# Performance work log

Hardware: AMD Instinct MI355X
Metric: run time of the kernel (lower is better)

Reference implementation:

```python
import jax, jax.numpy as jnp
import numpy as np

B, S, D, H, HID = 8192, 16, 128, 8, 1024
DH = D // H  # 16
GCN, NUMF = 40, 103
EPS = 1e-5

def _make_pe():
    pos = np.arange(S, dtype=np.float64)[:, None]
    i = np.arange(D, dtype=np.float64)[None, :]
    pe = pos / np.power(10000.0, (i // 2 * 2.0) / D)
    pe[:, 0::2] = np.sin(pe[:, 0::2])
    pe[:, 1::2] = np.cos(pe[:, 1::2])
    return jnp.asarray(pe, dtype=jnp.float32)  # [S, D]

PE = _make_pe()

def setup_inputs() -> dict:
    key = jax.random.key(0)
    ks = jax.random.split(key, 16)
    rn = lambda k, shape, s=0.02: (jax.random.normal(k, shape, jnp.float32) * s)
    return {
        "x": jax.random.normal(ks[0], (B, S, D), jnp.float32),
        "gcn_i": jax.random.normal(ks[1], (B, GCN), jnp.float32),
        "num": jax.random.normal(ks[2], (B, NUMF), jnp.float32),
        # two independent encoder layers, params stacked on leading dim
        "Wq": rn(ks[3], (2, D, D)), "bq": jnp.zeros((2, D), jnp.float32),
        "Wk": rn(ks[4], (2, D, D)), "bk": jnp.zeros((2, D), jnp.float32),
        "Wv": rn(ks[5], (2, D, D)), "bv": jnp.zeros((2, D), jnp.float32),
        "Wo": rn(ks[6], (2, D, D)), "bo": jnp.zeros((2, D), jnp.float32),
        "ln1_g": jnp.ones((2, D), jnp.float32), "ln1_b": jnp.zeros((2, D), jnp.float32),
        "W1": rn(ks[7], (2, D, HID)), "b1": jnp.zeros((2, HID), jnp.float32),
        "W2": rn(ks[8], (2, HID, D)), "b2": jnp.zeros((2, D), jnp.float32),
        "ln2_g": jnp.ones((2, D), jnp.float32), "ln2_b": jnp.zeros((2, D), jnp.float32),
        # head
        "Wn": rn(ks[9], (NUMF, D)), "bnum": jnp.zeros((D,), jnp.float32),
        "bn_gamma": jnp.ones((D,), jnp.float32), "bn_beta": jnp.zeros((D,), jnp.float32),
        "Wf": rn(ks[10], (S * D + GCN + D, 1)), "bf": jnp.zeros((1,), jnp.float32),
    }

def _ln(x, g, b):
    m = x.mean(-1, keepdims=True)
    v = ((x - m) ** 2).mean(-1, keepdims=True)
    return (x - m) * jax.lax.rsqrt(v + EPS) * g + b

def reference(x, gcn_i, num, Wq, bq, Wk, bk, Wv, bv, Wo, bo, ln1_g, ln1_b,
              W1, b1, W2, b2, ln2_g, ln2_b, Wn, bnum, bn_gamma, bn_beta, Wf, bf):
    out = x + PE  # positional encoding (dropout = identity in eval)
    scale = DH ** -0.5
    for l in range(2):
        # NOTE: original uses a raw .view(B*H, -1, DH) (no transpose) -- faithful reshape
        q = (out @ Wq[l] + bq[l]).reshape(B * H, S, DH)
        k = (out @ Wk[l] + bk[l]).reshape(B * H, S, DH)
        v = (out @ Wv[l] + bv[l]).reshape(B * H, S, DH)
        attn = jax.nn.softmax(jnp.einsum('nsd,ntd->nst', q, k) * scale, axis=-1)
        ctx = jnp.einsum('nst,ntd->nsd', attn, v).reshape(B, S, D)
        h = _ln(ctx @ Wo[l] + bo[l] + out, ln1_g[l], ln1_b[l])
        ff = jax.nn.relu(h @ W1[l] + b1[l]) @ W2[l] + b2[l]
        out = _ln(ff + h, ln2_g[l], ln2_b[l])
    flat = out.reshape(B, S * D)  # [B, 2048]
    n = num @ Wn + bnum  # [B, 128]
    # BatchNorm1d, training-mode forward (biased batch variance)
    mu = n.mean(0)
    var = ((n - mu) ** 2).mean(0)
    n = (n - mu) * jax.lax.rsqrt(var + EPS) * bn_gamma + bn_beta
    p = jnp.concatenate([flat, gcn_i, n], axis=-1)  # [B, 2216]
    return jax.nn.sigmoid(p @ Wf + bf)
```

## Files before the change

kernel.cpp:

```cpp
#include <hip/hip_runtime.h>
#include <hip/hip_bf16.h>
#include <math.h>

#define B_SZ   8192
#define S_SZ   16
#define D_SZ   128
#define HID_SZ 1024
#define NUMF_SZ 103
#define GCN_SZ 40
#define G_B    4
#define NBLK   (B_SZ / G_B)
#define STRD   136

typedef short bh8 __attribute__((ext_vector_type(8)));
typedef float fx4 __attribute__((ext_vector_type(4)));
typedef unsigned short us4 __attribute__((ext_vector_type(4)));

__device__ __forceinline__ fx4 mfma16(bh8 a, bh8 b, fx4 c) {
    return __builtin_amdgcn_mfma_f32_16x16x32_bf16(a, b, c, 0, 0, 0);
}

__device__ __forceinline__ unsigned short f2b(float f) {
    union { __hip_bfloat16 b; unsigned short u; } cv;
    cv.b = __float2bfloat16(f);
    return cv.u;
}
__device__ __forceinline__ float bu2f(unsigned short u) {
    return __uint_as_float(((unsigned)u) << 16);
}

__global__ __launch_bounds__(256) void prep_weights(
    const float* __restrict__ Wq, const float* __restrict__ Wk,
    const float* __restrict__ Wv, const float* __restrict__ Wo,
    const float* __restrict__ W1, const float* __restrict__ W2,
    unsigned short* __restrict__ WswQ, unsigned short* __restrict__ WswK,
    unsigned short* __restrict__ WswV, unsigned short* __restrict__ WswO,
    unsigned short* __restrict__ Wsw1, unsigned short* __restrict__ Wsw2,
    float* __restrict__ PEt)
{
    int i = blockIdx.x * 256 + threadIdx.x;
    if (i < 2048) {
        int s = i >> 7, c = i & 127;
        float expo = (float)((c >> 1) * 2) * (1.0f / 128.0f);
        float denom = powf(10000.0f, expo);
        float ang = (float)s / denom;
        PEt[i] = (c & 1) ? cosf(ang) : sinf(ang);
    }
    if (i < 2 * 16384) {
        int l = i >> 14, r = i & 16383;
        int nt = r >> 11, ks = (r >> 9) & 3, lane = (r >> 3) & 63, e = r & 7;
        int k = ks * 32 + (lane >> 4) * 8 + e;
        int n = nt * 16 + (lane & 15);
        int s = l * 16384 + k * 128 + n;
        WswQ[i] = f2b(Wq[s]); WswK[i] = f2b(Wk[s]);
        WswV[i] = f2b(Wv[s]); WswO[i] = f2b(Wo[s]);
    }
    {
        int l = i >> 17, r = i & 131071;
        int nt = r >> 11, ks = (r >> 9) & 3, lane = (r >> 3) & 63, e = r & 7;
        int k = ks * 32 + (lane >> 4) * 8 + e;
        int n = nt * 16 + (lane & 15);
        Wsw1[i] = f2b(W1[l * 131072 + k * 1024 + n]);
    }
    {
        int l = i >> 17, r = i & 131071;
        int nt = r >> 14, kt = (r >> 9) & 31, lane = (r >> 3) & 63, e = r & 7;
        int k = kt * 32 + (lane >> 4) * 8 + e;
        int n = nt * 16 + (lane & 15);
        Wsw2[i] = f2b(W2[l * 131072 + k * 128 + n]);
    }
}

__global__ __launch_bounds__(256, 2) void encoder_fused(
    const float* __restrict__ x, const float* __restrict__ gcn,
    const float* __restrict__ bq, const float* __restrict__ bk,
    const float* __restrict__ bv, const float* __restrict__ bo,
    const float* __restrict__ ln1g, const float* __restrict__ ln1b,
    const float* __restrict__ b1, const float* __restrict__ b2p,
    const float* __restrict__ ln2g, const float* __restrict__ ln2b,
    const float* __restrict__ Wf,
    const unsigned short* __restrict__ WswQ, const unsigned short* __restrict__ WswK,
    const unsigned short* __restrict__ WswV, const unsigned short* __restrict__ WswO,
    const unsigned short* __restrict__ Wsw1, const unsigned short* __restrict__ Wsw2,
    const float* __restrict__ PEt,
    float* __restrict__ acc1)
{
    __shared__ unsigned short ACT[64][STRD];
    __shared__ unsigned short Qb[64][STRD];
    __shared__ unsigned short Kb[64][STRD];
    __shared__ unsigned short Vb[64][STRD];
    __shared__ float2 LNp2[64][4];
    __shared__ float LNs[64][2];
    __shared__ unsigned short Pb[4][16][16];

    unsigned short* Vb4 = &Vb[0][0];

    const int t = threadIdx.x;
    const int w = t >> 6, lane = t & 63;
    const int q = lane >> 4, ln = lane & 15;
    const int bbase = blockIdx.x * G_B;

    {
        const float4* xb = (const float4*)(x + (size_t)bbase * 2048);
        const float4* pe4 = (const float4*)PEt;
#pragma unroll
        for (int i = 0; i < 8; ++i) {
            int f4 = i * 256 + t;
            float4 xv = xb[f4];
            float4 pv = pe4[f4 & 511];
            int flat = f4 * 4;
            int row = flat >> 7, col = flat & 127;
            ushort4 pk = {f2b(xv.x + pv.x), f2b(xv.y + pv.y),
                          f2b(xv.z + pv.z), f2b(xv.w + pv.w)};
            *(ushort4*)&ACT[row][col] = pk;
        }
    }
    __syncthreads();

    for (int l = 0; l < 2; ++l) {
        {
            bh8 afr[4][4];
#pragma unroll
            for (int mt = 0; mt < 4; ++mt)
#pragma unroll
                for (int ks = 0; ks < 4; ++ks)
                    afr[mt][ks] = *(const bh8*)&ACT[mt * 16 + ln][ks * 32 + q * 8];
#pragma unroll
            for (int mtx = 0; mtx < 2; ++mtx) {
                const unsigned short* Wm = (mtx == 0) ? WswQ + l * 16384 : WswK + l * 16384;
                const float* bias = (mtx == 0) ? bq + l * 128 : bk + l * 128;
                unsigned short (*dst)[STRD] = (mtx == 0) ? Qb : Kb;
#pragma unroll
                for (int i2 = 0; i2 < 2; ++i2) {
                    int nt = w * 2 + i2;
                    bh8 wfr[4];
#pragma unroll
                    for (int ks = 0; ks < 4; ++ks)
                        wfr[ks] = *(const bh8*)(Wm + ((nt * 4 + ks) * 64 + lane) * 8);
                    int n0 = nt * 16 + q * 4;
                    fx4 bb4 = *(const fx4*)&bias[n0];
#pragma unroll
                    for (int mt = 0; mt < 4; ++mt) {
                        fx4 acc = {0.f, 0.f, 0.f, 0.f};
#pragma unroll
                        for (int ks = 0; ks < 4; ++ks) acc = mfma16(wfr[ks], afr[mt][ks], acc);
                        us4 o;
#pragma unroll
                        for (int r2 = 0; r2 < 4; ++r2) o[r2] = f2b(acc[r2] + bb4[r2]);
                        *(us4*)&dst[mt * 16 + ln][n0] = o;
                    }
                }
            }
#pragma unroll
            for (int i2 = 0; i2 < 2; ++i2) {
                int nt = w * 2 + i2;
                bh8 wfr[4];
#pragma unroll
                for (int ks = 0; ks < 4; ++ks)
                    wfr[ks] = *(const bh8*)(WswV + l * 16384 + ((nt * 4 + ks) * 64 + lane) * 8);
                int n = nt * 16 + ln;
                float bb = bv[l * 128 + n];
#pragma unroll
                for (int mt = 0; mt < 4; ++mt) {
                    fx4 acc = {0.f, 0.f, 0.f, 0.f};
#pragma unroll
                    for (int ks = 0; ks < 4; ++ks) acc = mfma16(afr[mt][ks], wfr[ks], acc);
#pragma unroll
                    for (int r2 = 0; r2 < 4; ++r2) {
                        int s = q * 4 + r2;
                        Vb4[(((mt * 8 + (s >> 1)) * 16) + ln) * 16 +
                            (((s & 1) << 3) | nt)] = f2b(acc[r2] + bb);
                    }
                }
            }
        }
        __syncthreads();

        {
            const int E = w;
            const int rbase = E * 16 + (ln >> 3);
            const int ccol = (ln & 7) * 16;
#pragma unroll
            for (int g = 0; g < 8; ++g) {
                bh8 kfr = 0, qfr = 0;
                if (q < 2) {
                    kfr = *(const bh8*)&Kb[rbase + 2 * g][ccol + q * 8];
                    qfr = *(const bh8*)&Qb[rbase + 2 * g][ccol + q * 8];
                }
                fx4 st = mfma16(kfr, qfr, fx4{0.f, 0.f, 0.f, 0.f});
                float p0 = st[0] * 0.25f, p1 = st[1] * 0.25f;
                float p2 = st[2] * 0.25f, p3 = st[3] * 0.25f;
                float mx = fmaxf(fmaxf(p0, p1), fmaxf(p2, p3));
                mx = fmaxf(mx, __shfl_xor(mx, 16));
                mx = fmaxf(mx, __shfl_xor(mx, 32));
                p0 = __expf(p0 - mx); p1 = __expf(p1 - mx);
                p2 = __expf(p2 - mx); p3 = __expf(p3 - mx);
                float sm = (p0 + p1) + (p2 + p3);
                sm += __shfl_xor(sm, 16);
                sm += __shfl_xor(sm, 32);
                float is = 1.0f / sm;
                ushort4 pk = {f2b(p0 * is), f2b(p1 * is), f2b(p2 * is), f2b(p3 * is)};
                *(ushort4*)&Pb[w][ln][q * 4] = pk;
                bh8 vfr = 0, pfr = 0;
                if (q < 2) {
                    vfr = *(const bh8*)&Vb4[(((E * 8 + g) * 16) + ln) * 16 + q * 8];
                    pfr = *(const bh8*)&Pb[w][ln][q * 8];
                }
                fx4 cx = mfma16(vfr, pfr, fx4{0.f, 0.f, 0.f, 0.f});
                ushort4 ck = {f2b(cx[0]), f2b(cx[1]), f2b(cx[2]), f2b(cx[3])};
                *(ushort4*)&Qb[rbase + 2 * g][ccol + q * 4] = ck;
            }
        }
        __syncthreads();

        fx4 Cv[2][4];
        {
            bh8 cfr[4][4];
#pragma unroll
            for (int mt = 0; mt < 4; ++mt)
#pragma unroll
                for (int ks = 0; ks < 4; ++ks)
                    cfr[mt][ks] = *(const bh8*)&Qb[mt * 16 + ln][ks * 32 + q * 8];
#pragma unroll
            for (int i2 = 0; i2 < 2; ++i2) {
                int nt = w * 2 + i2, n0 = nt * 16 + q * 4;
                bh8 wfr[4];
#pragma unroll
                for (int ks = 0; ks < 4; ++ks)
                    wfr[ks] = *(const bh8*)(WswO + l * 16384 + ((nt * 4 + ks) * 64 + lane) * 8);
                fx4 bb4 = *(const fx4*)&bo[l * 128 + n0];
#pragma unroll
                for (int mt = 0; mt < 4; ++mt) {
                    fx4 acc = {0.f, 0.f, 0.f, 0.f};
#pragma unroll
                    for (int ks = 0; ks < 4; ++ks) acc = mfma16(wfr[ks], cfr[mt][ks], acc);
                    us4 rv = *(const us4*)&ACT[mt * 16 + ln][n0];
#pragma unroll
                    for (int r2 = 0; r2 < 4; ++r2)
                        Cv[i2][mt][r2] = acc[r2] + bb4[r2] + bu2f(rv[r2]);
                }
            }
        }
#pragma unroll
        for (int mt = 0; mt < 4; ++mt) {
            float s = 0.f, v = 0.f;
#pragma unroll
            for (int i2 = 0; i2 < 2; ++i2)
#pragma unroll
                for (int r2 = 0; r2 < 4; ++r2) {
                    float a = Cv[i2][mt][r2];
                    s += a; v = fmaf(a, a, v);
                }
            s += __shfl_xor(s, 16); v += __shfl_xor(v, 16);
            s += __shfl_xor(s, 32); v += __shfl_xor(v, 32);
            if (lane < 16) LNp2[mt * 16 + ln][w] = float2{s, v};
        }
        __syncthreads();
        if (t < 64) {
            float2 a0 = LNp2[t][0], a1 = LNp2[t][1];
            float2 a2 = LNp2[t][2], a3 = LNp2[t][3];
            float s = (a0.x + a1.x) + (a2.x + a3.x);
            float v = (a0.y + a1.y) + (a2.y + a3.y);
            float mean = s * (1.0f / 128.0f);
            LNs[t][0] = mean;
            LNs[t][1] = rsqrtf(v * (1.0f / 128.0f) - mean * mean + 1e-5f);
        }
        __syncthreads();
#pragma unroll
        for (int i2 = 0; i2 < 2; ++i2) {
            int n0 = (w * 2 + i2) * 16 + q * 4;
            fx4 gg = *(const fx4*)&ln1g[l * 128 + n0];
            fx4 be = *(const fx4*)&ln1b[l * 128 + n0];
#pragma unroll
            for (int mt = 0; mt < 4; ++mt) {
                int row = mt * 16 + ln;
                float mean = LNs[row][0], inv = LNs[row][1];
                us4 o;
#pragma unroll
                for (int r2 = 0; r2 < 4; ++r2)
                    o[r2] = f2b((Cv[i2][mt][r2] - mean) * inv * gg[r2] + be[r2]);
                *(us4*)&Kb[row][n0] = o;
            }
        }
        __syncthreads();

        bh8 hfr[4][4];
#pragma unroll
        for (int mt = 0; mt < 4; ++mt)
#pragma unroll
            for (int ks = 0; ks < 4; ++ks)
                hfr[mt][ks] = *(const bh8*)&Kb[mt * 16 + ln][ks * 32 + q * 8];
        fx4 f2a[2][4];
#pragma unroll
        for (int i2 = 0; i2 < 2; ++i2)
#pragma unroll
            for (int mt = 0; mt < 4; ++mt) f2a[i2][mt] = fx4{0.f, 0.f, 0.f, 0.f};
        for (int ch = 0; ch < 8; ++ch) {
            unsigned short (*dst)[STRD] = (ch & 1) ? Vb : Qb;
            bh8 w1fr[2][4];
#pragma unroll
            for (int i2 = 0; i2 < 2; ++i2) {
                int ntg = ch * 8 + w * 2 + i2;
#pragma unroll
                for (int ks = 0; ks < 4; ++ks)
                    w1fr[i2][ks] = *(const bh8*)(Wsw1 + l * 131072 + ((ntg * 4 + ks) * 64 + lane) * 8);
            }
#pragma unroll
            for (int mt = 0; mt < 4; ++mt) {
#pragma unroll
                for (int i2 = 0; i2 < 2; ++i2) {
                    fx4 acc = {0.f, 0.f, 0.f, 0.f};
#pragma unroll
                    for (int ks = 0; ks < 4; ++ks) acc = mfma16(w1fr[i2][ks], hfr[mt][ks], acc);
                    int nl0 = (w * 2 + i2) * 16 + q * 4;
                    fx4 bb4 = *(const fx4*)&b1[l * HID_SZ + ch * 128 + nl0];
                    us4 o;
#pragma unroll
                    for (int r2 = 0; r2 < 4; ++r2) {
                        float vv = acc[r2] + bb4[r2];
                        o[r2] = f2b(vv > 0.f ? vv : 0.f);
                    }
                    *(us4*)&dst[mt * 16 + ln][nl0] = o;
                }
            }
            __syncthreads();
            bh8 w2fr[2][4];
#pragma unroll
            for (int i2 = 0; i2 < 2; ++i2)
#pragma unroll
                for (int ks = 0; ks < 4; ++ks)
                    w2fr[i2][ks] = *(const bh8*)(Wsw2 + l * 131072 +
                        (((w * 2 + i2) * 32 + ch * 4 + ks) * 64 + lane) * 8);
#pragma unroll
            for (int mt = 0; mt < 4; ++mt) {
                bh8 ffr[4];
#pragma unroll
                for (int ks = 0; ks < 4; ++ks)
                    ffr[ks] = *(const bh8*)&dst[mt * 16 + ln][ks * 32 + q * 8];
#pragma unroll
                for (int i2 = 0; i2 < 2; ++i2)
#pragma unroll
                    for (int ks = 0; ks < 4; ++ks)
                        f2a[i2][mt] = mfma16(w2fr[i2][ks], ffr[ks], f2a[i2][mt]);
            }
        }
        fx4 Cv2[2][4];
#pragma unroll
        for (int i2 = 0; i2 < 2; ++i2) {
            int n0 = (w * 2 + i2) * 16 + q * 4;
            fx4 bb4 = *(const fx4*)&b2p[l * 128 + n0];
#pragma unroll
            for (int mt = 0; mt < 4; ++mt) {
                us4 rv = *(const us4*)&Kb[mt * 16 + ln][n0];
#pragma unroll
                for (int r2 = 0; r2 < 4; ++r2)
                    Cv2[i2][mt][r2] = f2a[i2][mt][r2] + bb4[r2] + bu2f(rv[r2]);
            }
        }
#pragma unroll
        for (int mt = 0; mt < 4; ++mt) {
            float s = 0.f, v = 0.f;
#pragma unroll
            for (int i2 = 0; i2 < 2; ++i2)
#pragma unroll
                for (int r2 = 0; r2 < 4; ++r2) {
                    float a = Cv2[i2][mt][r2];
                    s += a; v = fmaf(a, a, v);
                }
            s += __shfl_xor(s, 16); v += __shfl_xor(v, 16);
            s += __shfl_xor(s, 32); v += __shfl_xor(v, 32);
            if (lane < 16) LNp2[mt * 16 + ln][w] = float2{s, v};
        }
        __syncthreads();
        if (t < 64) {
            float2 a0 = LNp2[t][0], a1 = LNp2[t][1];
            float2 a2 = LNp2[t][2], a3 = LNp2[t][3];
            float s = (a0.x + a1.x) + (a2.x + a3.x);
            float v = (a0.y + a1.y) + (a2.y + a3.y);
            float mean = s * (1.0f / 128.0f);
            LNs[t][0] = mean;
            LNs[t][1] = rsqrtf(v * (1.0f / 128.0f) - mean * mean + 1e-5f);
        }
        __syncthreads();
#pragma unroll
        for (int i2 = 0; i2 < 2; ++i2) {
            int n0 = (w * 2 + i2) * 16 + q * 4;
            fx4 gg = *(const fx4*)&ln2g[l * 128 + n0];
            fx4 be = *(const fx4*)&ln2b[l * 128 + n0];
#pragma unroll
            for (int mt = 0; mt < 4; ++mt) {
                int row = mt * 16 + ln;
                float mean = LNs[row][0], inv = LNs[row][1];
                us4 o;
#pragma unroll
                for (int r2 = 0; r2 < 4; ++r2)
                    o[r2] = f2b((Cv2[i2][mt][r2] - mean) * inv * gg[r2] + be[r2]);
                *(us4*)&ACT[row][n0] = o;
            }
        }
        __syncthreads();
    }

    {
        int bg = bbase + w;
        float part = 0.f;
        int srow = lane >> 2, c0 = (lane & 3) * 32;
#pragma unroll
        for (int i = 0; i < 4; ++i) {
            bh8 av = *(const bh8*)&ACT[w * 16 + srow][c0 + i * 8];
            int fl = srow * 128 + c0 + i * 8;
#pragma unroll
            for (int e = 0; e < 8; ++e)
                part = fmaf(bu2f((unsigned short)av[e]), Wf[fl + e], part);
        }
        if (lane < GCN_SZ)
            part = fmaf(gcn[(size_t)bg * GCN_SZ + lane], Wf[2048 + lane], part);
#pragma unroll
        for (int off = 32; off; off >>= 1) part += __shfl_xor(part, off);
        if (lane == 0) acc1[bg] = part;
    }
}

__global__ __launch_bounds__(256) void num_stats_kernel(
    const float* __restrict__ num, const float* __restrict__ Wn,
    const float* __restrict__ bnum,
    float* __restrict__ ssum, float* __restrict__ ssq,
    float* __restrict__ nws, int have_nws)
{
    __shared__ float NUM[16][NUMF_SZ + 1];
    __shared__ float cred[4][128];
    const int t = threadIdx.x;
    const int b0 = blockIdx.x * 16;
    const int j = t & 127, sg = t >> 7, s0 = sg * 8;

    for (int idx = t; idx < 16 * NUMF_SZ; idx += 256) {
        int r = idx / NUMF_SZ, f = idx - r * NUMF_SZ;
        NUM[r][f] = num[(size_t)(b0 + r) * NUMF_SZ + f];
    }
    __syncthreads();

    float acc[8];
    float bnv = bnum[j];
#pragma unroll
    for (int r = 0; r < 8; ++r) acc[r] = bnv;
    for (int f = 0; f < NUMF_SZ; ++f) {
        float w = Wn[f * 128 + j];
#pragma unroll
        for (int r = 0; r < 8; ++r) acc[r] = fmaf(NUM[s0 + r][f], w, acc[r]);
    }
    if (have_nws) {
#pragma unroll
        for (int r = 0; r < 8; ++r)
            nws[(size_t)(b0 + s0 + r) * 128 + j] = acc[r];
    }
    float lsum = 0.f, lsq = 0.f;
#pragma unroll
    for (int r = 0; r < 8; ++r) {
        lsum += acc[r];
        lsq = fmaf(acc[r], acc[r], lsq);
    }
    cred[sg][j] = lsum;
    cred[2 + sg][j] = lsq;
    __syncthreads();
    if (sg == 0) atomicAdd(&ssum[j], cred[0][j] + cred[1][j]);
    else         atomicAdd(&ssq[j],  cred[2][j] + cred[3][j]);
}

__global__ __launch_bounds__(128) void bn_coef_kernel(
    const float* __restrict__ ssum, const float* __restrict__ ssq,
    const float* __restrict__ gamma, const float* __restrict__ beta,
    const float* __restrict__ Wf, const float* __restrict__ bfin,
    float* __restrict__ cvec)
{
    const int j = threadIdx.x;
    __shared__ float red2[2];
    float mean = ssum[j] * (1.0f / (float)B_SZ);
    float var = ssq[j] * (1.0f / (float)B_SZ) - mean * mean;
    float inv = rsqrtf(var + 1e-5f);
    float wj = Wf[2088 + j];
    float gi = gamma[j] * inv;
    cvec[j] = gi * wj;
    float k = (beta[j] - mean * gi) * wj;
#pragma unroll
    for (int o = 32; o; o >>= 1) k += __shfl_down(k, o);
    if ((j & 63) == 0) red2[j >> 6] = k;
    __syncthreads();
    if (j == 0) cvec[128] = red2[0] + red2[1] + bfin[0];
}

__global__ __launch_bounds__(256) void final_fast(
    const float* __restrict__ nws, const float* __restrict__ cvec,
    const float* __restrict__ acc1, float* __restrict__ out)
{
    __shared__ float cs[129];
    const int t = threadIdx.x;
    if (t < 129) cs[t] = cvec[t];
    __syncthreads();
    const int w = t >> 6, lane = t & 63;
    const int b = blockIdx.x * 4 + w;
    const float2* nb = (const float2*)(nws + (size_t)b * 128);
    float2 v = nb[lane];
    float d = v.x * cs[2 * lane] + v.y * cs[2 * lane + 1];
#pragma unroll
    for (int o = 32; o; o >>= 1) d += __shfl_xor(d, o);
    if (lane == 0)
        out[b] = 1.0f / (1.0f + __expf(-(acc1[b] + d + cs[128])));
}

__global__ __launch_bounds__(128) void final_kernel(
    const float* __restrict__ num, const float* __restrict__ Wn,
    const float* __restrict__ bnum,
    const float* __restrict__ ssum, const float* __restrict__ ssq,
    const float* __restrict__ gamma, const float* __restrict__ beta,
    const float* __restrict__ Wf, const float* __restrict__ bfin,
    const float* __restrict__ acc1, float* __restrict__ out)
{
    const int b = blockIdx.x, jj = threadIdx.x;
    __shared__ float red2[2];
    __shared__ float NUMr[NUMF_SZ];
    if (jj < NUMF_SZ) NUMr[jj] = num[(size_t)b * NUMF_SZ + jj];
    __syncthreads();
    float nv = bnum[jj];
    for (int f = 0; f < NUMF_SZ; ++f)
        nv = fmaf(NUMr[f], Wn[f * 128 + jj], nv);
    float mean = ssum[jj] * (1.0f / (float)B_SZ);
    float var = ssq[jj] * (1.0f / (float)B_SZ) - mean * mean;
    float bnv = (nv - mean) * rsqrtf(var + 1e-5f) * gamma[jj] + beta[jj];
    float v = bnv * Wf[2088 + jj];
#pragma unroll
    for (int o = 32; o; o >>= 1) v += __shfl_down(v, o);
    if ((jj & 63) == 0) red2[jj >> 6] = v;
    __syncthreads();
    if (jj == 0) {
        float z = acc1[b] + red2[0] + red2[1] + bfin[0];
        out[b] = 1.0f / (1.0f + __expf(-z));
    }
}

extern "C" void kernel_launch(void* const* d_in, const int* in_sizes, int n_in,
                              void* d_out, int out_size, void* d_ws, size_t ws_size,
                              hipStream_t stream)
{
    const float* x    = (const float*)d_in[0];
    const float* gcn  = (const float*)d_in[1];
    const float* num  = (const float*)d_in[2];
    const float* Wq   = (const float*)d_in[3];
    const float* bq   = (const float*)d_in[4];
    const float* Wk   = (const float*)d_in[5];
    const float* bk   = (const float*)d_in[6];
    const float* Wv   = (const float*)d_in[7];
    const float* bv   = (const float*)d_in[8];
    const float* Wo   = (const float*)d_in[9];
    const float* bo   = (const float*)d_in[10];
    const float* ln1g = (const float*)d_in[11];
    const float* ln1b = (const float*)d_in[12];
    const float* W1   = (const float*)d_in[13];
    const float* b1   = (const float*)d_in[14];
    const float* W2   = (const float*)d_in[15];
    const float* b2p  = (const float*)d_in[16];
    const float* ln2g = (const float*)d_in[17];
    const float* ln2b = (const float*)d_in[18];
    const float* Wn   = (const float*)d_in[19];
    const float* bnum = (const float*)d_in[20];
    const float* bng  = (const float*)d_in[21];
    const float* bnb  = (const float*)d_in[22];
    const float* Wf   = (const float*)d_in[23];
    const float* bfin = (const float*)d_in[24];

    float* acc1 = (float*)d_ws;
    float* ssum = acc1 + B_SZ;
    float* ssq  = ssum + 128;
    unsigned short* wb = (unsigned short*)((char*)d_ws + 40960);
    unsigned short* WswQ = wb;
    unsigned short* WswK = wb + 32768;
    unsigned short* WswV = wb + 65536;
    unsigned short* WswO = wb + 98304;
    unsigned short* Wsw1 = wb + 131072;
    unsigned short* Wsw2 = wb + 393216;
    float* PEt = (float*)((char*)d_ws + 40960 + 1310720);
    const size_t nws_off = 40960 + 1310720 + 8192;
    float* nws = (float*)((char*)d_ws + nws_off);
    const size_t cvec_off = nws_off + (size_t)B_SZ * 128 * sizeof(float);
    float* cvec = (float*)((char*)d_ws + cvec_off);
    const int have_nws = (ws_size >= cvec_off + 132 * sizeof(float)) ? 1 : 0;

    hipMemsetAsync(ssum, 0, 2 * 128 * sizeof(float), stream);
    prep_weights<<<1024, 256, 0, stream>>>(Wq, Wk, Wv, Wo, W1, W2,
        WswQ, WswK, WswV, WswO, Wsw1, Wsw2, PEt);
    encoder_fused<<<NBLK, 256, 0, stream>>>(x, gcn, bq, bk, bv, bo,
        ln1g, ln1b, b1, b2p, ln2g, ln2b, Wf,
        WswQ, WswK, WswV, WswO, Wsw1, Wsw2, PEt, acc1);
    num_stats_kernel<<<B_SZ / 16, 256, 0, stream>>>(num, Wn, bnum, ssum, ssq,
        nws, have_nws);
    if (have_nws) {
        bn_coef_kernel<<<1, 128, 0, stream>>>(ssum, ssq, bng, bnb, Wf, bfin, cvec);
        final_fast<<<B_SZ / 4, 256, 0, stream>>>(nws, cvec, acc1, (float*)d_out);
    } else {
        final_kernel<<<B_SZ, 128, 0, stream>>>(num, Wn, bnum, ssum, ssq, bng, bnb,
            Wf, bfin, acc1, (float*)d_out);
    }
}
```

Before: 402.8 us.

## Fold BatchNorm head into a 103-vector, drop nws buffer, inline LN stats

The BatchNorm head is linear after the statistics are known, so Wn·(gamma*inv*Wf) is folded into a 103-element coefficient vector plus a scalar. The final kernel then reads raw num rows instead of a stored 8192x128 intermediate, which removes that buffer's write and re-read and the fallback kernel. LayerNorm mean and rstd are now computed redundantly by every lane, which removes one barrier and a shared-memory stage per LayerNorm. The weight-prep kernel now reads source weights in coalesced order and scatters the writes instead.

```diff
diff --git a/kernel.cpp b/kernel.cpp
--- a/kernel.cpp
+++ b/kernel.cpp
@@ -38,36 +38,35 @@
     unsigned short* __restrict__ Wsw1, unsigned short* __restrict__ Wsw2,
     float* __restrict__ PEt)
 {
-    int i = blockIdx.x * 256 + threadIdx.x;
-    if (i < 2048) {
-        int s = i >> 7, c = i & 127;
+    int j = blockIdx.x * 256 + threadIdx.x;
+    if (j < 2048) {
+        int s = j >> 7, c = j & 127;
         float expo = (float)((c >> 1) * 2) * (1.0f / 128.0f);
         float denom = powf(10000.0f, expo);
         float ang = (float)s / denom;
-        PEt[i] = (c & 1) ? cosf(ang) : sinf(ang);
-    }
-    if (i < 2 * 16384) {
-        int l = i >> 14, r = i & 16383;
-        int nt = r >> 11, ks = (r >> 9) & 3, lane = (r >> 3) & 63, e = r & 7;
-        int k = ks * 32 + (lane >> 4) * 8 + e;
-        int n = nt * 16 + (lane & 15);
-        int s = l * 16384 + k * 128 + n;
-        WswQ[i] = f2b(Wq[s]); WswK[i] = f2b(Wk[s]);
-        WswV[i] = f2b(Wv[s]); WswO[i] = f2b(Wo[s]);
+        PEt[j] = (c & 1) ? cosf(ang) : sinf(ang);
+    }
+    if (j < 2 * 16384) {
+        int r = j & 16383, l = j >> 14;
+        int k = r >> 7, n = r & 127;
+        int dst = (((l * 8 + (n >> 4)) * 4 + (k >> 5)) * 64 +
+                   (((k >> 3) & 3) * 16 + (n & 15))) * 8 + (k & 7);
+        WswQ[dst] = f2b(Wq[j]); WswK[dst] = f2b(Wk[j]);
+        WswV[dst] = f2b(Wv[j]); WswO[dst] = f2b(Wo[j]);
     }
     {
-        int l = i >> 17, r = i & 131071;
-        int nt = r >> 11, ks = (r >> 9) & 3, lane = (r >> 3) & 63, e = r & 7;
-        int k = ks * 32 + (lane >> 4) * 8 + e;
-        int n = nt * 16 + (lane & 15);
-        Wsw1[i] = f2b(W1[l * 131072 + k * 1024 + n]);
+        int l = j >> 17, r = j & 131071;
+        int k = r >> 10, n = r & 1023;
+        int dst = (((l * 64 + (n >> 4)) * 4 + (k >> 5)) * 64 +
+                   (((k >> 3) & 3) * 16 + (n & 15))) * 8 + (k & 7);
+        Wsw1[dst] = f2b(W1[j]);
     }
     {
-        int l = i >> 17, r = i & 131071;
-        int nt = r >> 14, kt = (r >> 9) & 31, lane = (r >> 3) & 63, e = r & 7;
-        int k = kt * 32 + (lane >> 4) * 8 + e;
-        int n = nt * 16 + (lane & 15);
-        Wsw2[i] = f2b(W2[l * 131072 + k * 128 + n]);
+        int l = j >> 17, r = j & 131071;
+        int k = r >> 7, n = r & 127;
+        int dst = (((l * 8 + (n >> 4)) * 32 + (k >> 5)) * 64 +
+                   (((k >> 3) & 3) * 16 + (n & 15))) * 8 + (k & 7);
+        Wsw2[dst] = f2b(W2[j]);
     }
 }
 
@@ -90,7 +89,6 @@
     __shared__ unsigned short Kb[64][STRD];
     __shared__ unsigned short Vb[64][STRD];
     __shared__ float2 LNp2[64][4];
-    __shared__ float LNs[64][2];
     __shared__ unsigned short Pb[4][16][16];
 
     unsigned short* Vb4 = &Vb[0][0];
@@ -256,30 +254,32 @@
             if (lane < 16) LNp2[mt * 16 + ln][w] = float2{s, v};
         }
         __syncthreads();
-        if (t < 64) {
-            float2 a0 = LNp2[t][0], a1 = LNp2[t][1];
-            float2 a2 = LNp2[t][2], a3 = LNp2[t][3];
-            float s = (a0.x + a1.x) + (a2.x + a3.x);
-            float v = (a0.y + a1.y) + (a2.y + a3.y);
-            float mean = s * (1.0f / 128.0f);
-            LNs[t][0] = mean;
-            LNs[t][1] = rsqrtf(v * (1.0f / 128.0f) - mean * mean + 1e-5f);
-        }
-        __syncthreads();
-#pragma unroll
-        for (int i2 = 0; i2 < 2; ++i2) {
-            int n0 = (w * 2 + i2) * 16 + q * 4;
-            fx4 gg = *(const fx4*)&ln1g[l * 128 + n0];
-            fx4 be = *(const fx4*)&ln1b[l * 128 + n0];
+        {
+            float mean4[4], inv4[4];
 #pragma unroll
             for (int mt = 0; mt < 4; ++mt) {
                 int row = mt * 16 + ln;
-                float mean = LNs[row][0], inv = LNs[row][1];
-                us4 o;
-#pragma unroll
-                for (int r2 = 0; r2 < 4; ++r2)
-                    o[r2] = f2b((Cv[i2][mt][r2] - mean) * inv * gg[r2] + be[r2]);
-                *(us4*)&Kb[row][n0] = o;
+                float2 a0 = LNp2[row][0], a1 = LNp2[row][1];
+                float2 a2 = LNp2[row][2], a3 = LNp2[row][3];
+                float s = (a0.x + a1.x) + (a2.x + a3.x);
+                float v = (a0.y + a1.y) + (a2.y + a3.y);
+                float mean = s * (1.0f / 128.0f);
+                mean4[mt] = mean;
+                inv4[mt] = rsqrtf(v * (1.0f / 128.0f) - mean * mean + 1e-5f);
+            }
+#pragma unroll
+            for (int i2 = 0; i2 < 2; ++i2) {
+                int n0 = (w * 2 + i2) * 16 + q * 4;
+                fx4 gg = *(const fx4*)&ln1g[l * 128 + n0];
+                fx4 be = *(const fx4*)&ln1b[l * 128 + n0];
+#pragma unroll
+                for (int mt = 0; mt < 4; ++mt) {
+                    us4 o;
+#pragma unroll
+                    for (int r2 = 0; r2 < 4; ++r2)
+                        o[r2] = f2b((Cv[i2][mt][r2] - mean4[mt]) * inv4[mt] * gg[r2] + be[r2]);
+                    *(us4*)&Kb[mt * 16 + ln][n0] = o;
+                }
             }
         }
         __syncthreads();
@@ -372,30 +372,32 @@
             if (lane < 16) LNp2[mt * 16 + ln][w] = float2{s, v};
         }
         __syncthreads();
-        if (t < 64) {
-            float2 a0 = LNp2[t][0], a1 = LNp2[t][1];
-            float2 a2 = LNp2[t][2], a3 = LNp2[t][3];
-            float s = (a0.x + a1.x) + (a2.x + a3.x);
-            float v = (a0.y + a1.y) + (a2.y + a3.y);
-            float mean = s * (1.0f / 128.0f);
-            LNs[t][0] = mean;
-            LNs[t][1] = rsqrtf(v * (1.0f / 128.0f) - mean * mean + 1e-5f);
-        }
-        __syncthreads();
-#pragma unroll
-        for (int i2 = 0; i2 < 2; ++i2) {
-            int n0 = (w * 2 + i2) * 16 + q * 4;
-            fx4 gg = *(const fx4*)&ln2g[l * 128 + n0];
-            fx4 be = *(const fx4*)&ln2b[l * 128 + n0];
+        {
+            float mean4[4], inv4[4];
 #pragma unroll
             for (int mt = 0; mt < 4; ++mt) {
                 int row = mt * 16 + ln;
-                float mean = LNs[row][0], inv = LNs[row][1];
-                us4 o;
-#pragma unroll
-                for (int r2 = 0; r2 < 4; ++r2)
-                    o[r2] = f2b((Cv2[i2][mt][r2] - mean) * inv * gg[r2] + be[r2]);
-                *(us4*)&ACT[row][n0] = o;
+                float2 a0 = LNp2[row][0], a1 = LNp2[row][1];
+                float2 a2 = LNp2[row][2], a3 = LNp2[row][3];
+                float s = (a0.x + a1.x) + (a2.x + a3.x);
+                float v = (a0.y + a1.y) + (a2.y + a3.y);
+                float mean = s * (1.0f / 128.0f);
+                mean4[mt] = mean;
+                inv4[mt] = rsqrtf(v * (1.0f / 128.0f) - mean * mean + 1e-5f);
+            }
+#pragma unroll
+            for (int i2 = 0; i2 < 2; ++i2) {
+                int n0 = (w * 2 + i2) * 16 + q * 4;
+                fx4 gg = *(const fx4*)&ln2g[l * 128 + n0];
+                fx4 be = *(const fx4*)&ln2b[l * 128 + n0];
+#pragma unroll
+                for (int mt = 0; mt < 4; ++mt) {
+                    us4 o;
+#pragma unroll
+                    for (int r2 = 0; r2 < 4; ++r2)
+                        o[r2] = f2b((Cv2[i2][mt][r2] - mean4[mt]) * inv4[mt] * gg[r2] + be[r2]);
+                    *(us4*)&ACT[mt * 16 + ln][n0] = o;
+                }
             }
         }
         __syncthreads();
@@ -424,8 +426,7 @@
 __global__ __launch_bounds__(256) void num_stats_kernel(
     const float* __restrict__ num, const float* __restrict__ Wn,
     const float* __restrict__ bnum,
-    float* __restrict__ ssum, float* __restrict__ ssq,
-    float* __restrict__ nws, int have_nws)
+    float* __restrict__ ssum, float* __restrict__ ssq)
 {
     __shared__ float NUM[16][NUMF_SZ + 1];
     __shared__ float cred[4][128];
@@ -448,11 +449,6 @@
 #pragma unroll
         for (int r = 0; r < 8; ++r) acc[r] = fmaf(NUM[s0 + r][f], w, acc[r]);
     }
-    if (have_nws) {
-#pragma unroll
-        for (int r = 0; r < 8; ++r)
-            nws[(size_t)(b0 + s0 + r) * 128 + j] = acc[r];
-    }
     float lsum = 0.f, lsq = 0.f;
 #pragma unroll
     for (int r = 0; r < 8; ++r) {
@@ -470,71 +466,50 @@
     const float* __restrict__ ssum, const float* __restrict__ ssq,
     const float* __restrict__ gamma, const float* __restrict__ beta,
     const float* __restrict__ Wf, const float* __restrict__ bfin,
+    const float* __restrict__ Wn, const float* __restrict__ bnum,
     float* __restrict__ cvec)
 {
     const int j = threadIdx.x;
+    __shared__ float cS[128];
     __shared__ float red2[2];
     float mean = ssum[j] * (1.0f / (float)B_SZ);
     float var = ssq[j] * (1.0f / (float)B_SZ) - mean * mean;
     float inv = rsqrtf(var + 1e-5f);
     float wj = Wf[2088 + j];
     float gi = gamma[j] * inv;
-    cvec[j] = gi * wj;
-    float k = (beta[j] - mean * gi) * wj;
+    float cj = gi * wj;
+    cS[j] = cj;
+    float k = (beta[j] - mean * gi) * wj + bnum[j] * cj;
 #pragma unroll
     for (int o = 32; o; o >>= 1) k += __shfl_down(k, o);
     if ((j & 63) == 0) red2[j >> 6] = k;
     __syncthreads();
-    if (j == 0) cvec[128] = red2[0] + red2[1] + bfin[0];
+    if (j == 0) cvec[103] = red2[0] + red2[1] + bfin[0];
+    if (j < NUMF_SZ) {
+        float s = 0.f;
+        for (int jj = 0; jj < 128; ++jj)
+            s = fmaf(Wn[j * 128 + jj], cS[jj], s);
+        cvec[j] = s;
+    }
 }
 
 __global__ __launch_bounds__(256) void final_fast(
-    const float* __restrict__ nws, const float* __restrict__ cvec,
+    const float* __restrict__ num, const float* __restrict__ cvec,
     const float* __restrict__ acc1, float* __restrict__ out)
 {
-    __shared__ float cs[129];
+    __shared__ float wv[104];
     const int t = threadIdx.x;
-    if (t < 129) cs[t] = cvec[t];
+    if (t < 104) wv[t] = cvec[t];
     __syncthreads();
     const int w = t >> 6, lane = t & 63;
     const int b = blockIdx.x * 4 + w;
-    const float2* nb = (const float2*)(nws + (size_t)b * 128);
-    float2 v = nb[lane];
-    float d = v.x * cs[2 * lane] + v.y * cs[2 * lane + 1];
-#pragma unroll
-    for (int o = 32; o; o >>= 1) d += __shfl_xor(d, o);
+    const float* nb = num + (size_t)b * NUMF_SZ;
+    float part = nb[lane] * wv[lane];
+    if (lane < NUMF_SZ - 64) part += nb[64 + lane] * wv[64 + lane];
+#pragma unroll
+    for (int o = 32; o; o >>= 1) part += __shfl_xor(part, o);
     if (lane == 0)
-        out[b] = 1.0f / (1.0f + __expf(-(acc1[b] + d + cs[128])));
-}
-
-__global__ __launch_bounds__(128) void final_kernel(
-    const float* __restrict__ num, const float* __restrict__ Wn,
-    const float* __restrict__ bnum,
-    const float* __restrict__ ssum, const float* __restrict__ ssq,
-    const float* __restrict__ gamma, const float* __restrict__ beta,
-    const float* __restrict__ Wf, const float* __restrict__ bfin,
-    const float* __restrict__ acc1, float* __restrict__ out)
-{
-    const int b = blockIdx.x, jj = threadIdx.x;
-    __shared__ float red2[2];
-    __shared__ float NUMr[NUMF_SZ];
-    if (jj < NUMF_SZ) NUMr[jj] = num[(size_t)b * NUMF_SZ + jj];
-    __syncthreads();
-    float nv = bnum[jj];
-    for (int f = 0; f < NUMF_SZ; ++f)
-        nv = fmaf(NUMr[f], Wn[f * 128 + jj], nv);
-    float mean = ssum[jj] * (1.0f / (float)B_SZ);
-    float var = ssq[jj] * (1.0f / (float)B_SZ) - mean * mean;
-    float bnv = (nv - mean) * rsqrtf(var + 1e-5f) * gamma[jj] + beta[jj];
-    float v = bnv * Wf[2088 + jj];
-#pragma unroll
-    for (int o = 32; o; o >>= 1) v += __shfl_down(v, o);
-    if ((jj & 63) == 0) red2[jj >> 6] = v;
-    __syncthreads();
-    if (jj == 0) {
-        float z = acc1[b] + red2[0] + red2[1] + bfin[0];
-        out[b] = 1.0f / (1.0f + __expf(-z));
-    }
+        out[b] = 1.0f / (1.0f + __expf(-(acc1[b] + part + wv[103])));
 }
 
 extern "C" void kernel_launch(void* const* d_in, const int* in_sizes, int n_in,
@@ -578,11 +553,7 @@
     unsigned short* Wsw1 = wb + 131072;
     unsigned short* Wsw2 = wb + 393216;
     float* PEt = (float*)((char*)d_ws + 40960 + 1310720);
-    const size_t nws_off = 40960 + 1310720 + 8192;
-    float* nws = (float*)((char*)d_ws + nws_off);
-    const size_t cvec_off = nws_off + (size_t)B_SZ * 128 * sizeof(float);
-    float* cvec = (float*)((char*)d_ws + cvec_off);
-    const int have_nws = (ws_size >= cvec_off + 132 * sizeof(float)) ? 1 : 0;
+    float* cvec = (float*)((char*)d_ws + 40960 + 1310720 + 8192);
 
     hipMemsetAsync(ssum, 0, 2 * 128 * sizeof(float), stream);
     prep_weights<<<1024, 256, 0, stream>>>(Wq, Wk, Wv, Wo, W1, W2,
@@ -590,13 +561,8 @@
     encoder_fused<<<NBLK, 256, 0, stream>>>(x, gcn, bq, bk, bv, bo,
         ln1g, ln1b, b1, b2p, ln2g, ln2b, Wf,
         WswQ, WswK, WswV, WswO, Wsw1, Wsw2, PEt, acc1);
-    num_stats_kernel<<<B_SZ / 16, 256, 0, stream>>>(num, Wn, bnum, ssum, ssq,
-        nws, have_nws);
-    if (have_nws) {
-        bn_coef_kernel<<<1, 128, 0, stream>>>(ssum, ssq, bng, bnb, Wf, bfin, cvec);
-        final_fast<<<B_SZ / 4, 256, 0, stream>>>(nws, cvec, acc1, (float*)d_out);
-    } else {
-        final_kernel<<<B_SZ, 128, 0, stream>>>(num, Wn, bnum, ssum, ssq, bng, bnb,
-            Wf, bfin, acc1, (float*)d_out);
-    }
-}
+    num_stats_kernel<<<B_SZ / 16, 256, 0, stream>>>(num, Wn, bnum, ssum, ssq);
+    bn_coef_kernel<<<1, 128, 0, stream>>>(ssum, ssq, bng, bnb, Wf, bfin,
+        Wn, bnum, cvec);
+    final_fast<<<B_SZ / 4, 256, 0, stream>>>(num, cvec, acc1, (float*)d_out);
+}
```

Measured after the change: 406.0 us. No clear change (+0.8%).
